# Kernel tuning notes

Hardware: AMD Instinct MI355X
Metric: run time of the kernel (lower is better)

## Reference

```python
import jax, jax.numpy as jnp
import numpy as np

N = 100000
E = 1600000
IN_CH = 128
HID = 16
HEADS = 4
OUT_CH = 2
EDGE_DIM = 3
NEG_SLOPE = 0.2


def gat_layer(x, src, dst, e_feat, W, att_src, att_dst, We, att_edge, bias, H, C, concat):
    # x: [N, Fin] -> projected [N, H, C]
    xs = (x @ W).reshape(-1, H, C)
    a_src = jnp.sum(xs * att_src, axis=-1)          # [N, H]
    a_dst = jnp.sum(xs * att_dst, axis=-1)          # [N, H]
    ee = (e_feat @ We).reshape(-1, H, C)            # [E, H, C]
    a_edge = jnp.sum(ee * att_edge, axis=-1)        # [E, H]
    alpha = a_src[src] + a_dst[dst] + a_edge        # [E, H]
    alpha = jax.nn.leaky_relu(alpha, NEG_SLOPE)
    # segment softmax over incoming edges of each dst node
    seg_max = jax.ops.segment_max(alpha, dst, num_segments=N)
    alpha = jnp.exp(alpha - seg_max[dst])
    seg_sum = jax.ops.segment_sum(alpha, dst, num_segments=N)
    alpha = alpha / (seg_sum[dst] + 1e-16)
    # weighted message aggregation
    msg = xs[src] * alpha[:, :, None]               # [E, H, C]
    out = jax.ops.segment_sum(msg, dst, num_segments=N)  # [N, H, C]
    out = out.reshape(-1, H * C) if concat else out.mean(axis=1)
    return out + bias


def setup_inputs() -> dict:
    key = jax.random.key(0)
    ks = jax.random.split(key, 24)
    g = lambda i, shape, scale=0.1: jax.random.normal(ks[i], shape, dtype=jnp.float32) * scale
    inp = {
        "x": jax.random.normal(ks[0], (N, IN_CH), dtype=jnp.float32),
        "edge_index": jax.random.randint(ks[1], (2, E), 0, N, dtype=jnp.int32),
        "edge_feat": jax.random.normal(ks[2], (E, EDGE_DIM), dtype=jnp.float32),
        # edge MLP
        "Em1": g(3, (EDGE_DIM, EDGE_DIM)), "eb1": g(4, (EDGE_DIM,)),
        "Em2": g(5, (EDGE_DIM, EDGE_DIM)), "eb2": g(6, (EDGE_DIM,)),
        # conv1: in -> HID per head, HEADS heads, concat
        "W1": g(7, (IN_CH, HEADS * HID)),
        "as1": g(8, (HEADS, HID)), "ad1": g(9, (HEADS, HID)),
        "We1": g(10, (EDGE_DIM, HEADS * HID)), "ae1": g(11, (HEADS, HID)),
        "b1": g(12, (HEADS * HID,)),
        # conv2: HEADS*HID -> OUT_CH, 1 head, no concat
        "W2": g(13, (HEADS * HID, OUT_CH)),
        "as2": g(14, (1, OUT_CH)), "ad2": g(15, (1, OUT_CH)),
        "We2": g(16, (EDGE_DIM, OUT_CH)), "ae2": g(17, (1, OUT_CH)),
        "b2": g(18, (OUT_CH,)),
    }
    return inp


def reference(x, edge_index, edge_feat,
              Em1, eb1, Em2, eb2,
              W1, as1, ad1, We1, ae1, b1,
              W2, as2, ad2, We2, ae2, b2):
    src, dst = edge_index[0], edge_index[1]
    # edge MLP: Linear -> ReLU -> Linear
    e = jax.nn.relu(edge_feat @ Em1 + eb1) @ Em2 + eb2
    # dropout layers are identity in eval mode
    h = gat_layer(x, src, dst, e, W1, as1, ad1, We1, ae1, b1, HEADS, HID, concat=True)
    h = jax.nn.elu(h)
    out = gat_layer(h, src, dst, e, W2, as2, ad2, We2, ae2, b2, 1, OUT_CH, concat=False)
    return out
```

## Files before the change

### kernel.cpp

```cpp
#include <hip/hip_runtime.h>
#include <hip/hip_fp16.h>
#include <math.h>
#include <stdint.h>

#define NEG_SLOPE 0.2f
#define SCAN_TILE 2048

__device__ __forceinline__ float leaky(float a) { return a > 0.f ? a : NEG_SLOPE * a; }
__device__ __forceinline__ __half2 u2h2(unsigned u) { return *reinterpret_cast<__half2*>(&u); }

__global__ __launch_bounds__(256) void k_pw(const int* __restrict__ dst, int* __restrict__ deg,
                                            int* __restrict__ pw, int E,
                                            const float* __restrict__ We1, const float* __restrict__ ae1,
                                            const float* __restrict__ We2, const float* __restrict__ ae2,
                                            float* __restrict__ cw) {
    if (blockIdx.x == 0 && threadIdx.x == 0) {
        for (int i = 0; i < 3; i++)
            for (int h = 0; h < 4; h++) {
                float s = 0.f;
                for (int m = 0; m < 16; m++) s += We1[i*64 + h*16 + m] * ae1[h*16 + m];
                cw[i*4 + h] = s;
            }
        for (int i = 0; i < 3; i++) cw[12 + i] = We2[i*2]*ae2[0] + We2[i*2+1]*ae2[1];
    }
    int base = (blockIdx.x * blockDim.x + threadIdx.x) * 4;
    if (base >= E) return;
    if (base + 3 < E) {
        int4 dv = *reinterpret_cast<const int4*>(&dst[base]);
        int4 pv;
        pv.x = atomicAdd(&deg[dv.x], 1);
        pv.y = atomicAdd(&deg[dv.y], 1);
        pv.z = atomicAdd(&deg[dv.z], 1);
        pv.w = atomicAdd(&deg[dv.w], 1);
        *reinterpret_cast<int4*>(&pw[base]) = pv;
    } else {
        for (int i = base; i < E; i++) pw[i] = atomicAdd(&deg[dst[i]], 1);
    }
}

__global__ __launch_bounds__(256) void k_scan_partial(const int* __restrict__ deg, int* __restrict__ tsum, int N) {
    __shared__ int sh[256];
    int b = blockIdx.x, t = threadIdx.x;
    int base = b * SCAN_TILE + t * 8;
    int s = 0;
    #pragma unroll
    for (int i = 0; i < 8; i++) { int idx = base + i; s += (idx < N) ? deg[idx] : 0; }
    sh[t] = s; __syncthreads();
    for (int o = 128; o > 0; o >>= 1) { if (t < o) sh[t] += sh[t + o]; __syncthreads(); }
    if (t == 0) tsum[b] = sh[0];
}

__global__ void k_scan_tsum(const int* __restrict__ tsum, int* __restrict__ toff,
                            int* __restrict__ rowptr, int nb, int N) {
    if (threadIdx.x == 0 && blockIdx.x == 0) {
        int run = 0;
        for (int i = 0; i < nb; i++) { toff[i] = run; run += tsum[i]; }
        rowptr[N] = run;
    }
}

__global__ __launch_bounds__(256) void k_scan_final(const int* __restrict__ deg, const int* __restrict__ toff,
        int* __restrict__ rowptr, int* __restrict__ cmbi, int N) {
    __shared__ int sh[256];
    int b = blockIdx.x, t = threadIdx.x;
    int base = b * SCAN_TILE + t * 8;
    int v[8]; int s = 0;
    #pragma unroll
    for (int i = 0; i < 8; i++) { int idx = base + i; v[i] = (idx < N) ? deg[idx] : 0; s += v[i]; }
    sh[t] = s; __syncthreads();
    for (int o = 1; o < 256; o <<= 1) {
        int u = (t >= o) ? sh[t - o] : 0;
        __syncthreads();
        sh[t] += u;
        __syncthreads();
    }
    int run = sh[t] - s + toff[b];
    #pragma unroll
    for (int i = 0; i < 8; i++) {
        int idx = base + i;
        if (idx < N) { rowptr[idx] = run; cmbi[(size_t)idx*8 + 4] = run; run += v[i]; }
    }
}

__global__ __launch_bounds__(256) void k_proj1(const float* __restrict__ x, const float* __restrict__ W1,
        const float* __restrict__ as1, const float* __restrict__ ad1,
        __half* __restrict__ xs1h, float* __restrict__ as1v, float* __restrict__ cmbf, int N) {
    __shared__ float xr[32][128];
    int tid = threadIdx.x;
    int wave = tid >> 6, lane = tid & 63;
    int nbase = blockIdx.x * 32;
    if (nbase + 32 <= N) {
        const float4* x4 = reinterpret_cast<const float4*>(x + (size_t)nbase * 128);
        #pragma unroll
        for (int i = 0; i < 4; i++) {
            int idx = tid + i * 256;
            reinterpret_cast<float4*>(&xr[0][0])[idx] = x4[idx];
        }
    } else {
        for (int i = 0; i < 16; i++) {
            int flat = tid + i * 256;
            int row = flat >> 7, col = flat & 127;
            int n = nbase + row; if (n >= N) n = N - 1;
            xr[row][col] = x[(size_t)n * 128 + col];
        }
    }
    __syncthreads();
    int cc = lane & 15, kk = lane >> 4;
    int nw = wave * 8;
    const float4* W4 = reinterpret_cast<const float4*>(W1);
    float4 acc[8];
    #pragma unroll
    for (int m = 0; m < 8; m++) acc[m] = make_float4(0.f, 0.f, 0.f, 0.f);
    #pragma unroll 4
    for (int k = kk; k < 128; k += 4) {
        float4 wv = W4[k * 16 + cc];
        #pragma unroll
        for (int m = 0; m < 8; m++) {
            float xv = xr[nw + m][k];
            acc[m].x = fmaf(xv, wv.x, acc[m].x);
            acc[m].y = fmaf(xv, wv.y, acc[m].y);
            acc[m].z = fmaf(xv, wv.z, acc[m].z);
            acc[m].w = fmaf(xv, wv.w, acc[m].w);
        }
    }
    float a_s0 = as1[4*cc], a_s1 = as1[4*cc+1], a_s2 = as1[4*cc+2], a_s3 = as1[4*cc+3];
    float a_d0 = ad1[4*cc], a_d1 = ad1[4*cc+1], a_d2 = ad1[4*cc+2], a_d3 = ad1[4*cc+3];
    #pragma unroll
    for (int m = 0; m < 8; m++) {
        float4 a = acc[m];
        a.x += __shfl_xor(a.x, 16, 64); a.y += __shfl_xor(a.y, 16, 64);
        a.z += __shfl_xor(a.z, 16, 64); a.w += __shfl_xor(a.w, 16, 64);
        a.x += __shfl_xor(a.x, 32, 64); a.y += __shfl_xor(a.y, 32, 64);
        a.z += __shfl_xor(a.z, 32, 64); a.w += __shfl_xor(a.w, 32, 64);
        float ps = a.x*a_s0 + a.y*a_s1 + a.z*a_s2 + a.w*a_s3;
        float pd = a.x*a_d0 + a.y*a_d1 + a.z*a_d2 + a.w*a_d3;
        ps += __shfl_xor(ps, 1, 64); ps += __shfl_xor(ps, 2, 64);
        pd += __shfl_xor(pd, 1, 64); pd += __shfl_xor(pd, 2, 64);
        if (kk == 0) {
            int n = nbase + nw + m; if (n >= N) n = N - 1;
            __half2 h01 = __halves2half2(__float2half_rn(a.x), __float2half_rn(a.y));
            __half2 h23 = __halves2half2(__float2half_rn(a.z), __float2half_rn(a.w));
            uint2 st;
            st.x = *reinterpret_cast<unsigned*>(&h01);
            st.y = *reinterpret_cast<unsigned*>(&h23);
            *reinterpret_cast<uint2*>(&xs1h[(size_t)n*64 + 4*cc]) = st;
            if ((cc & 3) == 0) {
                int h = cc >> 2;
                as1v[n*4 + h] = ps;
                cmbf[(size_t)n*8 + h] = pd;
            }
        }
    }
}

__global__ __launch_bounds__(256) void k_payload(const float* __restrict__ ef,
                       const float* __restrict__ Em1, const float* __restrict__ eb1,
                       const float* __restrict__ Em2, const float* __restrict__ eb2,
                       const float* __restrict__ cw,
                       const int* __restrict__ src, const int* __restrict__ dst,
                       const int* __restrict__ pw,
                       const float4* __restrict__ as1v4,
                       const float* __restrict__ cmbf, const int* __restrict__ cmbi,
                       uint4* __restrict__ csr_pk, int E) {
    int base = (blockIdx.x * blockDim.x + threadIdx.x) * 4;
    if (base >= E) return;
    int cnt = min(4, E - base);

    float f[4][3]; int sv[4], dv[4], pv[4];
    if (cnt == 4) {
        const float4* ef4 = reinterpret_cast<const float4*>(ef);
        float4 a = ef4[base*3/4 + 0], b = ef4[base*3/4 + 1], c = ef4[base*3/4 + 2];
        f[0][0]=a.x; f[0][1]=a.y; f[0][2]=a.z;
        f[1][0]=a.w; f[1][1]=b.x; f[1][2]=b.y;
        f[2][0]=b.z; f[2][1]=b.w; f[2][2]=c.x;
        f[3][0]=c.y; f[3][1]=c.z; f[3][2]=c.w;
        int4 s4 = *reinterpret_cast<const int4*>(&src[base]);
        int4 d4 = *reinterpret_cast<const int4*>(&dst[base]);
        int4 p4 = *reinterpret_cast<const int4*>(&pw[base]);
        sv[0]=s4.x; sv[1]=s4.y; sv[2]=s4.z; sv[3]=s4.w;
        dv[0]=d4.x; dv[1]=d4.y; dv[2]=d4.z; dv[3]=d4.w;
        pv[0]=p4.x; pv[1]=p4.y; pv[2]=p4.z; pv[3]=p4.w;
    } else {
        for (int i = 0; i < cnt; i++) {
            f[i][0]=ef[(base+i)*3+0]; f[i][1]=ef[(base+i)*3+1]; f[i][2]=ef[(base+i)*3+2];
            sv[i]=src[base+i]; dv[i]=dst[base+i]; pv[i]=pw[base+i];
        }
    }

    #pragma unroll
    for (int i = 0; i < 4; i++) {
        if (i >= cnt) break;
        float f0=f[i][0], f1=f[i][1], f2=f[i][2];
        float t0 = fmaxf(f0*Em1[0]+f1*Em1[3]+f2*Em1[6]+eb1[0], 0.f);
        float t1 = fmaxf(f0*Em1[1]+f1*Em1[4]+f2*Em1[7]+eb1[1], 0.f);
        float t2 = fmaxf(f0*Em1[2]+f1*Em1[5]+f2*Em1[8]+eb1[2], 0.f);
        float u0 = t0*Em2[0]+t1*Em2[3]+t2*Em2[6]+eb2[0];
        float u1 = t0*Em2[1]+t1*Em2[4]+t2*Em2[7]+eb2[1];
        float u2 = t0*Em2[2]+t1*Em2[5]+t2*Em2[8]+eb2[2];
        int s = sv[i], d = dv[i];
        float4 av = as1v4[s];
        float4 bv = *reinterpret_cast<const float4*>(&cmbf[(size_t)d*8]);
        int rp = cmbi[(size_t)d*8 + 4];
        float w0 = __expf(leaky(av.x + bv.x + u0*cw[0] + u1*cw[4] + u2*cw[8]));
        float w1 = __expf(leaky(av.y + bv.y + u0*cw[1] + u1*cw[5] + u2*cw[9]));
        float w2 = __expf(leaky(av.z + bv.z + u0*cw[2] + u1*cw[6] + u2*cw[10]));
        float w3 = __expf(leaky(av.w + bv.w + u0*cw[3] + u1*cw[7] + u2*cw[11]));
        float e2 = u0*cw[12] + u1*cw[13] + u2*cw[14];
        __half2 lo = __halves2half2(__float2half_rn(w0), __float2half_rn(w1));
        __half2 hi = __halves2half2(__float2half_rn(w2), __float2half_rn(w3));
        uint4 pki;
        pki.x = (unsigned)s;
        pki.y = *reinterpret_cast<unsigned*>(&lo);
        pki.z = *reinterpret_cast<unsigned*>(&hi);
        pki.w = *reinterpret_cast<unsigned*>(&e2);
        csr_pk[rp + pv[i]] = pki;
    }
}

__global__ __launch_bounds__(256, 4) void k_gat1(
        const int* __restrict__ rowptr, const uint4* __restrict__ csr_pk,
        const __half* __restrict__ xs1h,
        const float* __restrict__ b1, const float* __restrict__ W2,
        const float* __restrict__ as2, const float* __restrict__ ad2,
        float2* __restrict__ pk2, float* __restrict__ ad2v, int N) {
    int wave = threadIdx.x >> 6, lane = threadIdx.x & 63;
    int d = blockIdx.x * 4 + wave;
    if (d >= N) return;
    int beg = rowptr[d], end = rowptr[d+1];
    int cg = lane & 15, e4 = lane >> 4;
    int hh = cg >> 2;
    const __half* xbase = xs1h + 4 * cg;
    float4 acc = make_float4(0.f, 0.f, 0.f, 0.f);
    float4 wv  = make_float4(0.f, 0.f, 0.f, 0.f);
    for (int off = beg; off < end; off += 16) {
        int j = off + cg;
        uint4 p = make_uint4(0u, 0u, 0u, 0u);
        if (j < end) p = csr_pk[j];
        int si = (int)p.x;
        __half2 wl = u2h2(p.y), whp = u2h2(p.z);
        wv.x += __low2float(wl);  wv.y += __high2float(wl);
        wv.z += __low2float(whp); wv.w += __high2float(whp);
        int st0, st1, st2, st3; float wt0, wt1, wt2, wt3;
        {
            int sl0 = 0*4 + e4, sl1 = 1*4 + e4, sl2 = 2*4 + e4, sl3 = 3*4 + e4;
            st0 = __shfl(si, sl0, 16); st1 = __shfl(si, sl1, 16);
            st2 = __shfl(si, sl2, 16); st3 = __shfl(si, sl3, 16);
            unsigned y0 = __shfl(p.y, sl0, 16), z0 = __shfl(p.z, sl0, 16);
            unsigned y1 = __shfl(p.y, sl1, 16), z1 = __shfl(p.z, sl1, 16);
            unsigned y2 = __shfl(p.y, sl2, 16), z2 = __shfl(p.z, sl2, 16);
            unsigned y3 = __shfl(p.y, sl3, 16), z3 = __shfl(p.z, sl3, 16);
            unsigned q0 = (hh < 2) ? y0 : z0;
            unsigned q1 = (hh < 2) ? y1 : z1;
            unsigned q2 = (hh < 2) ? y2 : z2;
            unsigned q3 = (hh < 2) ? y3 : z3;
            wt0 = (hh & 1) ? __high2float(u2h2(q0)) : __low2float(u2h2(q0));
            wt1 = (hh & 1) ? __high2float(u2h2(q1)) : __low2float(u2h2(q1));
            wt2 = (hh & 1) ? __high2float(u2h2(q2)) : __low2float(u2h2(q2));
            wt3 = (hh & 1) ? __high2float(u2h2(q3)) : __low2float(u2h2(q3));
        }
        uint2 g0 = *reinterpret_cast<const uint2*>(xbase + ((size_t)st0 << 6));
        uint2 g1 = *reinterpret_cast<const uint2*>(xbase + ((size_t)st1 << 6));
        uint2 g2 = *reinterpret_cast<const uint2*>(xbase + ((size_t)st2 << 6));
        uint2 g3 = *reinterpret_cast<const uint2*>(xbase + ((size_t)st3 << 6));
        __half2 a, b;
        a = u2h2(g0.x); b = u2h2(g0.y);
        acc.x = fmaf(wt0, __low2float(a), acc.x); acc.y = fmaf(wt0, __high2float(a), acc.y);
        acc.z = fmaf(wt0, __low2float(b), acc.z); acc.w = fmaf(wt0, __high2float(b), acc.w);
        a = u2h2(g1.x); b = u2h2(g1.y);
        acc.x = fmaf(wt1, __low2float(a), acc.x); acc.y = fmaf(wt1, __high2float(a), acc.y);
        acc.z = fmaf(wt1, __low2float(b), acc.z); acc.w = fmaf(wt1, __high2float(b), acc.w);
        a = u2h2(g2.x); b = u2h2(g2.y);
        acc.x = fmaf(wt2, __low2float(a), acc.x); acc.y = fmaf(wt2, __high2float(a), acc.y);
        acc.z = fmaf(wt2, __low2float(b), acc.z); acc.w = fmaf(wt2, __high2float(b), acc.w);
        a = u2h2(g3.x); b = u2h2(g3.y);
        acc.x = fmaf(wt3, __low2float(a), acc.x); acc.y = fmaf(wt3, __high2float(a), acc.y);
        acc.z = fmaf(wt3, __low2float(b), acc.z); acc.w = fmaf(wt3, __high2float(b), acc.w);
    }
    acc.x += __shfl_xor(acc.x, 16, 64); acc.y += __shfl_xor(acc.y, 16, 64);
    acc.z += __shfl_xor(acc.z, 16, 64); acc.w += __shfl_xor(acc.w, 16, 64);
    acc.x += __shfl_xor(acc.x, 32, 64); acc.y += __shfl_xor(acc.y, 32, 64);
    acc.z += __shfl_xor(acc.z, 32, 64); acc.w += __shfl_xor(acc.w, 32, 64);
    #pragma unroll
    for (int o = 1; o <= 8; o <<= 1) {
        wv.x += __shfl_xor(wv.x, o, 16); wv.y += __shfl_xor(wv.y, o, 16);
        wv.z += __shfl_xor(wv.z, o, 16); wv.w += __shfl_xor(wv.w, o, 16);
    }
    float sm = (hh == 0) ? wv.x : (hh == 1) ? wv.y : (hh == 2) ? wv.z : wv.w;
    float inv = 1.f / (sm + 1e-16f);
    float v0 = acc.x * inv + b1[4*cg + 0];
    float v1 = acc.y * inv + b1[4*cg + 1];
    float v2 = acc.z * inv + b1[4*cg + 2];
    float v3 = acc.w * inv + b1[4*cg + 3];
    v0 = v0 > 0.f ? v0 : expm1f(v0);
    v1 = v1 > 0.f ? v1 : expm1f(v1);
    v2 = v2 > 0.f ? v2 : expm1f(v2);
    v3 = v3 > 0.f ? v3 : expm1f(v3);
    float p0 = v0*W2[(4*cg+0)*2] + v1*W2[(4*cg+1)*2] + v2*W2[(4*cg+2)*2] + v3*W2[(4*cg+3)*2];
    float p1 = v0*W2[(4*cg+0)*2+1] + v1*W2[(4*cg+1)*2+1] + v2*W2[(4*cg+2)*2+1] + v3*W2[(4*cg+3)*2+1];
    #pragma unroll
    for (int o = 1; o <= 8; o <<= 1) { p0 += __shfl_xor(p0, o, 16); p1 += __shfl_xor(p1, o, 16); }
    if (lane == 0) {
        float2 q;
        q.x = p0*as2[0] + p1*as2[1];
        __half2 xv = __halves2half2(__float2half_rn(p0), __float2half_rn(p1));
        q.y = *reinterpret_cast<float*>(&xv);
        pk2[d] = q;
        ad2v[d] = p0*ad2[0] + p1*ad2[1];
    }
}

__global__ __launch_bounds__(256) void k_gat2(
        const int* __restrict__ rowptr, const uint4* __restrict__ csr_pk,
        const float2* __restrict__ pk2, const float* __restrict__ ad2v,
        const float* __restrict__ b2, float* __restrict__ out, int N) {
    int t = blockIdx.x * blockDim.x + threadIdx.x;
    int d = t >> 4, j16 = t & 15;
    if (d >= N) return;
    int beg = rowptr[d], end = rowptr[d+1];
    float add = ad2v[d];
    float sm = 0.f, p0 = 0.f, p1 = 0.f;
    for (int off = beg; off < end; off += 16) {
        int j = off + j16;
        if (j < end) {
            uint4 p = csr_pk[j];
            int s = (int)p.x;
            float ea2 = *reinterpret_cast<float*>(&p.w);
            float2 q = pk2[s];
            float w = __expf(leaky(q.x + add + ea2));
            __half2 xv = *reinterpret_cast<__half2*>(&q.y);
            p0 = fmaf(w, __low2float(xv), p0);
            p1 = fmaf(w, __high2float(xv), p1);
            sm += w;
        }
    }
    #pragma unroll
    for (int o = 1; o < 16; o <<= 1) {
        sm += __shfl_xor(sm, o, 16);
        p0 += __shfl_xor(p0, o, 16);
        p1 += __shfl_xor(p1, o, 16);
    }
    if (j16 == 0) {
        float inv = 1.f / (sm + 1e-16f);
        out[d*2+0] = p0*inv + b2[0];
        out[d*2+1] = p1*inv + b2[1];
    }
}

extern "C" void kernel_launch(void* const* d_in, const int* in_sizes, int n_in,
                              void* d_out, int out_size, void* d_ws, size_t ws_size,
                              hipStream_t stream) {
    const float* x   = (const float*)d_in[0];
    const int*   ei  = (const int*)d_in[1];
    const float* ef  = (const float*)d_in[2];
    const float* Em1 = (const float*)d_in[3];
    const float* eb1 = (const float*)d_in[4];
    const float* Em2 = (const float*)d_in[5];
    const float* eb2 = (const float*)d_in[6];
    const float* W1  = (const float*)d_in[7];
    const float* as1 = (const float*)d_in[8];
    const float* ad1 = (const float*)d_in[9];
    const float* We1 = (const float*)d_in[10];
    const float* ae1 = (const float*)d_in[11];
    const float* b1  = (const float*)d_in[12];
    const float* W2  = (const float*)d_in[13];
    const float* as2 = (const float*)d_in[14];
    const float* ad2 = (const float*)d_in[15];
    const float* We2 = (const float*)d_in[16];
    const float* ae2 = (const float*)d_in[17];
    const float* b2  = (const float*)d_in[18];

    const int N = in_sizes[0] / 128;
    const int E = in_sizes[1] / 2;
    const int* srcp = ei;
    const int* dstp = ei + E;

    uintptr_t w = (uintptr_t)d_ws;
    auto alloc = [&](size_t bytes) -> void* {
        uintptr_t p = w; w += (bytes + 255) & ~(size_t)255; return (void*)p;
    };
    const int nb = (N + SCAN_TILE - 1) / SCAN_TILE;
    int*    deg     = (int*)alloc((size_t)N * sizeof(int));
    int*    rowptr  = (int*)alloc(((size_t)N + 1) * sizeof(int));
    int*    tsum    = (int*)alloc((size_t)nb * sizeof(int));
    int*    toff    = (int*)alloc((size_t)(nb + 1) * sizeof(int));
    float*  cw      = (float*)alloc(16 * sizeof(float));
    int*    pw      = (int*)alloc((size_t)E * sizeof(int));
    uint4*  csr_pk  = (uint4*)alloc((size_t)E * sizeof(uint4));
    __half* xs1h    = (__half*)alloc((size_t)N * 64 * sizeof(__half));
    float*  as1v    = (float*)alloc((size_t)N * 4 * sizeof(float));
    float*  cmb     = (float*)alloc((size_t)N * 8 * sizeof(float));
    float2* pk2     = (float2*)alloc((size_t)N * sizeof(float2));
    float*  ad2v    = (float*)alloc((size_t)N * sizeof(float));

    const int B = 256;

    hipMemsetAsync(deg, 0, (size_t)N * sizeof(int), stream);
    k_pw<<<(E/4+B-1)/B + 1, B, 0, stream>>>(dstp, deg, pw, E, We1, ae1, We2, ae2, cw);
    k_scan_partial<<<nb, 256, 0, stream>>>(deg, tsum, N);
    k_scan_tsum<<<1, 64, 0, stream>>>(tsum, toff, rowptr, nb, N);
    k_scan_final<<<nb, 256, 0, stream>>>(deg, toff, rowptr, (int*)cmb, N);
    k_proj1<<<(N+31)/32, 256, 0, stream>>>(x, W1, as1, ad1, xs1h, as1v, cmb, N);
    k_payload<<<(E/4+B-1)/B + 1, B, 0, stream>>>(ef, Em1, eb1, Em2, eb2, cw,
                                                 srcp, dstp, pw, (const float4*)as1v,
                                                 cmb, (const int*)cmb, csr_pk, E);
    k_gat1<<<(N+3)/4, 256, 0, stream>>>(rowptr, csr_pk, xs1h, b1, W2, as2, ad2, pk2, ad2v, N);
    k_gat2<<<(N*16+B-1)/B, B, 0, stream>>>(rowptr, csr_pk, pk2, ad2v, b2, (float*)d_out, N);
}
```

Before: 251.5 us.

## Split degree counters into eight block-sharded copies to reduce atomic contention

The degree histogram is replicated eight times, indexed by block id modulo eight, and each edge's slot index is tagged with its shard in the top bits. The scan kernels sum across shards, and per-node per-shard offsets are stored in a widened combined node record so the payload kernel can compute the CSR slot. The aim is to spread same-address atomics across separate counters. In exchange it adds an eight-times larger memset, extra scan reads, and a 64-byte node record in place of the 32-byte one, which means more gather traffic in the payload kernel.

```diff
diff --git a/kernel.cpp b/kernel.cpp
--- a/kernel.cpp
+++ b/kernel.cpp
@@ -9,8 +9,8 @@
 __device__ __forceinline__ float leaky(float a) { return a > 0.f ? a : NEG_SLOPE * a; }
 __device__ __forceinline__ __half2 u2h2(unsigned u) { return *reinterpret_cast<__half2*>(&u); }
 
-__global__ __launch_bounds__(256) void k_pw(const int* __restrict__ dst, int* __restrict__ deg,
-                                            int* __restrict__ pw, int E,
+__global__ __launch_bounds__(256) void k_pw(const int* __restrict__ dst, int* __restrict__ deg8,
+                                            int* __restrict__ pw, int E, int N,
                                             const float* __restrict__ We1, const float* __restrict__ ae1,
                                             const float* __restrict__ We2, const float* __restrict__ ae2,
                                             float* __restrict__ cw) {
@@ -23,28 +23,39 @@
             }
         for (int i = 0; i < 3; i++) cw[12 + i] = We2[i*2]*ae2[0] + We2[i*2+1]*ae2[1];
     }
+    int c = blockIdx.x & 7;
+    int* deg = deg8 + (size_t)c * N;
+    unsigned ctag = (unsigned)c << 28;
     int base = (blockIdx.x * blockDim.x + threadIdx.x) * 4;
     if (base >= E) return;
     if (base + 3 < E) {
         int4 dv = *reinterpret_cast<const int4*>(&dst[base]);
         int4 pv;
-        pv.x = atomicAdd(&deg[dv.x], 1);
-        pv.y = atomicAdd(&deg[dv.y], 1);
-        pv.z = atomicAdd(&deg[dv.z], 1);
-        pv.w = atomicAdd(&deg[dv.w], 1);
+        pv.x = atomicAdd(&deg[dv.x], 1) | ctag;
+        pv.y = atomicAdd(&deg[dv.y], 1) | ctag;
+        pv.z = atomicAdd(&deg[dv.z], 1) | ctag;
+        pv.w = atomicAdd(&deg[dv.w], 1) | ctag;
         *reinterpret_cast<int4*>(&pw[base]) = pv;
     } else {
-        for (int i = base; i < E; i++) pw[i] = atomicAdd(&deg[dst[i]], 1);
-    }
-}
-
-__global__ __launch_bounds__(256) void k_scan_partial(const int* __restrict__ deg, int* __restrict__ tsum, int N) {
+        for (int i = base; i < E; i++) pw[i] = atomicAdd(&deg[dst[i]], 1) | ctag;
+    }
+}
+
+__global__ __launch_bounds__(256) void k_scan_partial(const int* __restrict__ deg8, int* __restrict__ tsum, int N) {
     __shared__ int sh[256];
     int b = blockIdx.x, t = threadIdx.x;
     int base = b * SCAN_TILE + t * 8;
     int s = 0;
-    #pragma unroll
-    for (int i = 0; i < 8; i++) { int idx = base + i; s += (idx < N) ? deg[idx] : 0; }
+    if (base + 8 <= N) {
+        for (int c = 0; c < 8; c++) {
+            const int4* p4 = reinterpret_cast<const int4*>(deg8 + (size_t)c * N + base);
+            int4 a = p4[0], bb = p4[1];
+            s += a.x + a.y + a.z + a.w + bb.x + bb.y + bb.z + bb.w;
+        }
+    } else if (base < N) {
+        for (int i = base; i < N; i++)
+            for (int c = 0; c < 8; c++) s += deg8[(size_t)c * N + i];
+    }
     sh[t] = s; __syncthreads();
     for (int o = 128; o > 0; o >>= 1) { if (t < o) sh[t] += sh[t + o]; __syncthreads(); }
     if (t == 0) tsum[b] = sh[0];
@@ -59,14 +70,21 @@
     }
 }
 
-__global__ __launch_bounds__(256) void k_scan_final(const int* __restrict__ deg, const int* __restrict__ toff,
+__global__ __launch_bounds__(256) void k_scan_final(const int* __restrict__ deg8, const int* __restrict__ toff,
         int* __restrict__ rowptr, int* __restrict__ cmbi, int N) {
     __shared__ int sh[256];
     int b = blockIdx.x, t = threadIdx.x;
     int base = b * SCAN_TILE + t * 8;
-    int v[8]; int s = 0;
-    #pragma unroll
-    for (int i = 0; i < 8; i++) { int idx = base + i; v[i] = (idx < N) ? deg[idx] : 0; s += v[i]; }
+    int vt[8]; int s = 0;
+    #pragma unroll
+    for (int i = 0; i < 8; i++) {
+        int idx = base + i; int tot = 0;
+        if (idx < N) {
+            #pragma unroll
+            for (int c = 0; c < 8; c++) tot += deg8[(size_t)c * N + idx];
+        }
+        vt[i] = tot; s += tot;
+    }
     sh[t] = s; __syncthreads();
     for (int o = 1; o < 256; o <<= 1) {
         int u = (t >= o) ? sh[t - o] : 0;
@@ -78,7 +96,16 @@
     #pragma unroll
     for (int i = 0; i < 8; i++) {
         int idx = base + i;
-        if (idx < N) { rowptr[idx] = run; cmbi[(size_t)idx*8 + 4] = run; run += v[i]; }
+        if (idx < N) {
+            rowptr[idx] = run;
+            int off = run;
+            #pragma unroll
+            for (int c = 0; c < 8; c++) {
+                cmbi[(size_t)idx * 16 + 4 + c] = off;
+                off += deg8[(size_t)c * N + idx];
+            }
+            run += vt[i];
+        }
     }
 }
 
@@ -147,7 +174,7 @@
             if ((cc & 3) == 0) {
                 int h = cc >> 2;
                 as1v[n*4 + h] = ps;
-                cmbf[(size_t)n*8 + h] = pd;
+                cmbf[(size_t)n*16 + h] = pd;
             }
         }
     }
@@ -199,8 +226,10 @@
         float u2 = t0*Em2[2]+t1*Em2[5]+t2*Em2[8]+eb2[2];
         int s = sv[i], d = dv[i];
         float4 av = as1v4[s];
-        float4 bv = *reinterpret_cast<const float4*>(&cmbf[(size_t)d*8]);
-        int rp = cmbi[(size_t)d*8 + 4];
+        float4 bv = *reinterpret_cast<const float4*>(&cmbf[(size_t)d*16]);
+        int c  = ((unsigned)pv[i]) >> 28;
+        int ps = pv[i] & 0x0FFFFFFF;
+        int slot = cmbi[(size_t)d*16 + 4 + c] + ps;
         float w0 = __expf(leaky(av.x + bv.x + u0*cw[0] + u1*cw[4] + u2*cw[8]));
         float w1 = __expf(leaky(av.y + bv.y + u0*cw[1] + u1*cw[5] + u2*cw[9]));
         float w2 = __expf(leaky(av.z + bv.z + u0*cw[2] + u1*cw[6] + u2*cw[10]));
@@ -213,7 +242,7 @@
         pki.y = *reinterpret_cast<unsigned*>(&lo);
         pki.z = *reinterpret_cast<unsigned*>(&hi);
         pki.w = *reinterpret_cast<unsigned*>(&e2);
-        csr_pk[rp + pv[i]] = pki;
+        csr_pk[slot] = pki;
     }
 }
 
@@ -379,7 +408,7 @@
         uintptr_t p = w; w += (bytes + 255) & ~(size_t)255; return (void*)p;
     };
     const int nb = (N + SCAN_TILE - 1) / SCAN_TILE;
-    int*    deg     = (int*)alloc((size_t)N * sizeof(int));
+    int*    deg8    = (int*)alloc((size_t)8 * N * sizeof(int));
     int*    rowptr  = (int*)alloc(((size_t)N + 1) * sizeof(int));
     int*    tsum    = (int*)alloc((size_t)nb * sizeof(int));
     int*    toff    = (int*)alloc((size_t)(nb + 1) * sizeof(int));
@@ -388,17 +417,17 @@
     uint4*  csr_pk  = (uint4*)alloc((size_t)E * sizeof(uint4));
     __half* xs1h    = (__half*)alloc((size_t)N * 64 * sizeof(__half));
     float*  as1v    = (float*)alloc((size_t)N * 4 * sizeof(float));
-    float*  cmb     = (float*)alloc((size_t)N * 8 * sizeof(float));
+    float*  cmb     = (float*)alloc((size_t)N * 16 * sizeof(float));
     float2* pk2     = (float2*)alloc((size_t)N * sizeof(float2));
     float*  ad2v    = (float*)alloc((size_t)N * sizeof(float));
 
     const int B = 256;
 
-    hipMemsetAsync(deg, 0, (size_t)N * sizeof(int), stream);
-    k_pw<<<(E/4+B-1)/B + 1, B, 0, stream>>>(dstp, deg, pw, E, We1, ae1, We2, ae2, cw);
-    k_scan_partial<<<nb, 256, 0, stream>>>(deg, tsum, N);
+    hipMemsetAsync(deg8, 0, (size_t)8 * N * sizeof(int), stream);
+    k_pw<<<(E/4+B-1)/B + 1, B, 0, stream>>>(dstp, deg8, pw, E, N, We1, ae1, We2, ae2, cw);
+    k_scan_partial<<<nb, 256, 0, stream>>>(deg8, tsum, N);
     k_scan_tsum<<<1, 64, 0, stream>>>(tsum, toff, rowptr, nb, N);
-    k_scan_final<<<nb, 256, 0, stream>>>(deg, toff, rowptr, (int*)cmb, N);
+    k_scan_final<<<nb, 256, 0, stream>>>(deg8, toff, rowptr, (int*)cmb, N);
     k_proj1<<<(N+31)/32, 256, 0, stream>>>(x, W1, as1, ad1, xs1h, as1v, cmb, N);
     k_payload<<<(E/4+B-1)/B + 1, B, 0, stream>>>(ef, Em1, eb1, Em2, eb2, cw,
                                                  srcp, dstp, pw, (const float4*)as1v,
```

Measured after the change: 269.2 us. 7.0% more time.
